# Performance work log

Hardware: AMD Instinct MI355X
Metric: run time of the kernel (lower is better)

## Reference

```python
import jax, jax.numpy as jnp
import numpy as np

DROPOUT = 0.1      # ban radius in normalized coords
INVALID = -2.0     # PositionGetter.INVALID sentinel
EPS = 1e-08


def setup_inputs() -> dict:
    key = jax.random.key(0)
    k1, k2, k3 = jax.random.split(key, 3)
    B, C, T, D = 64, 275, 3000, 2
    x = jax.random.normal(k1, (B, C, T), dtype=jnp.float32)
    positions = jax.random.uniform(k2, (B, C, D), dtype=jnp.float32)
    # row 0: the ban center applied to x; rows 1..100: Monte-Carlo test centers
    centers = jax.random.uniform(k3, (101, D), dtype=jnp.float32)
    return {"x": x, "positions": positions, "centers": centers}


def reference(x, positions, centers):
    # valid_mask: channel is valid unless all coords equal the INVALID sentinel
    valid = ~jnp.all(positions == INVALID, axis=-1)          # [B, C] bool
    x = x * valid[..., None].astype(x.dtype)
    # distances from every channel position to every center, all at once
    # centers: [N, D], positions: [B, C, D] -> dist: [N, B, C]
    diff = positions[None, :, :, :] - centers[:, None, None, :]
    dist = jnp.linalg.norm(diff, axis=-1)                    # [N, B, C]
    kept_all = (dist > DROPOUT) | (~valid)[None]             # [N, B, C] bool
    # apply the actual ban (first center)
    x = x * kept_all[0][..., None].astype(x.dtype)
    # Monte-Carlo keep probability over the remaining 100 centers
    prob_kept = jnp.mean(kept_all[1:].astype(x.dtype), axis=0)  # [B, C]
    return x / (prob_kept[..., None] + EPS)
```

## Files before the change

kernel.cpp:

```cpp
#include <hip/hip_runtime.h>
#include <math.h>


__global__ __launch_bounds__(256) void ChannelDropout_14851996910142_kernel(
    const float* __restrict__ x,
    const float* __restrict__ pos,
    const float* __restrict__ centers,
    float* __restrict__ out,
    int ncenters, int tlen)
{
    const int row = blockIdx.x;
    const int tid = threadIdx.x;
    __shared__ float s_scale;

    if (tid < 64) {
        const float px = pos[2 * row];
        const float py = pos[2 * row + 1];
        const bool valid = !(px == -2.0f && py == -2.0f);

        float cnt = 0.0f;
        for (int c = 1 + tid; c < ncenters; c += 64) {
            const float dx = px - centers[2 * c];
            const float dy = py - centers[2 * c + 1];
            const float d2 = __fadd_rn(__fmul_rn(dx, dx), __fmul_rn(dy, dy));
            const float d = sqrtf(d2);
            cnt += (d > 0.1f) ? 1.0f : 0.0f;
        }
        #pragma unroll
        for (int off = 32; off > 0; off >>= 1)
            cnt += __shfl_down(cnt, off, 64);

        if (tid == 0) {
            const float dx0 = px - centers[0];
            const float dy0 = py - centers[1];
            const float d02 = __fadd_rn(__fmul_rn(dx0, dx0), __fmul_rn(dy0, dy0));
            const bool kept0 = sqrtf(d02) > 0.1f;
            const float prob = cnt / (float)(ncenters - 1);
            s_scale = (valid && kept0) ? (1.0f / (prob + 1e-8f)) : 0.0f;
        }
    }
    __syncthreads();
    const float s = s_scale;

    const size_t base = (size_t)row * (size_t)tlen;
    const int t4 = tlen >> 2;
    const float4* __restrict__ xr = (const float4*)(x + base);
    float4* __restrict__ orow = (float4*)(out + base);
    for (int i = tid; i < t4; i += 256) {
        float4 v = xr[i];
        v.x *= s; v.y *= s; v.z *= s; v.w *= s;
        orow[i] = v;
    }
    for (int i = (t4 << 2) + tid; i < tlen; i += 256) {
        out[base + i] = x[base + i] * s;
    }
}

extern "C" void kernel_launch(void* const* d_in, const int* in_sizes, int n_in,
                              void* d_out, int out_size, void* d_ws, size_t ws_size,
                              hipStream_t stream) {
    const float* x       = (const float*)d_in[0];
    const float* pos     = (const float*)d_in[1];
    const float* centers = (const float*)d_in[2];
    float* out = (float*)d_out;

    const int rows     = in_sizes[1] / 2;
    const int tlen     = in_sizes[0] / rows;
    const int ncenters = in_sizes[2] / 2;

    ChannelDropout_14851996910142_kernel<<<rows, 256, 0, stream>>>(
        x, pos, centers, out, ncenters, tlen);
}
```

Baseline: 348.8 us.

## Split scale computation into separate kernel and use nontemporal streaming loads/stores

Per-row scale computation moves into a small pre-kernel where each thread handles one row and reads the centers from shared memory. The streaming kernel then only loads one precomputed scale per row, so the wave-level reduction and block barrier leave the bandwidth-bound loop. The loop also switches to nontemporal loads and stores to avoid polluting the cache. The cost is a second launch and a workspace round-trip, and the shared buffer caps centers at 256.

```diff
diff --git a/kernel.cpp b/kernel.cpp
--- a/kernel.cpp
+++ b/kernel.cpp
@@ -2,56 +2,63 @@
 #include <math.h>
 
 
-__global__ __launch_bounds__(256) void ChannelDropout_14851996910142_kernel(
-    const float* __restrict__ x,
+typedef float vfloat4 __attribute__((ext_vector_type(4)));
+
+#define MAX_CENTER_FLOATS 512
+
+__global__ __launch_bounds__(256) void ChannelDropout_scale_kernel(
     const float* __restrict__ pos,
     const float* __restrict__ centers,
+    float* __restrict__ scale,
+    int rows, int ncenters)
+{
+    __shared__ float sc[MAX_CENTER_FLOATS];
+    const int nfl = 2 * ncenters;
+    for (int i = threadIdx.x; i < nfl; i += 256) sc[i] = centers[i];
+    __syncthreads();
+
+    const int row = blockIdx.x * 256 + threadIdx.x;
+    if (row >= rows) return;
+
+    const float px = pos[2 * row];
+    const float py = pos[2 * row + 1];
+    const bool valid = !(px == -2.0f && py == -2.0f);
+
+    float cnt = 0.0f;
+    for (int c = 1; c < ncenters; ++c) {
+        const float dx = px - sc[2 * c];
+        const float dy = py - sc[2 * c + 1];
+        const float d = sqrtf(__fadd_rn(__fmul_rn(dx, dx), __fmul_rn(dy, dy)));
+        cnt += (d > 0.1f) ? 1.0f : 0.0f;
+    }
+    const float dx0 = px - sc[0];
+    const float dy0 = py - sc[1];
+    const bool kept0 =
+        sqrtf(__fadd_rn(__fmul_rn(dx0, dx0), __fmul_rn(dy0, dy0))) > 0.1f;
+    const float prob = cnt / (float)(ncenters - 1);
+    scale[row] = (valid && kept0) ? (1.0f / (prob + 1e-8f)) : 0.0f;
+}
+
+__global__ __launch_bounds__(256) void ChannelDropout_apply_kernel(
+    const float* __restrict__ x,
+    const float* __restrict__ scale,
     float* __restrict__ out,
-    int ncenters, int tlen)
+    int tlen)
 {
     const int row = blockIdx.x;
-    const int tid = threadIdx.x;
-    __shared__ float s_scale;
-
-    if (tid < 64) {
-        const float px = pos[2 * row];
-        const float py = pos[2 * row + 1];
-        const bool valid = !(px == -2.0f && py == -2.0f);
-
-        float cnt = 0.0f;
-        for (int c = 1 + tid; c < ncenters; c += 64) {
-            const float dx = px - centers[2 * c];
-            const float dy = py - centers[2 * c + 1];
-            const float d2 = __fadd_rn(__fmul_rn(dx, dx), __fmul_rn(dy, dy));
-            const float d = sqrtf(d2);
-            cnt += (d > 0.1f) ? 1.0f : 0.0f;
-        }
-        #pragma unroll
-        for (int off = 32; off > 0; off >>= 1)
-            cnt += __shfl_down(cnt, off, 64);
-
-        if (tid == 0) {
-            const float dx0 = px - centers[0];
-            const float dy0 = py - centers[1];
-            const float d02 = __fadd_rn(__fmul_rn(dx0, dx0), __fmul_rn(dy0, dy0));
-            const bool kept0 = sqrtf(d02) > 0.1f;
-            const float prob = cnt / (float)(ncenters - 1);
-            s_scale = (valid && kept0) ? (1.0f / (prob + 1e-8f)) : 0.0f;
-        }
-    }
-    __syncthreads();
-    const float s = s_scale;
+    const float s = scale[row];
 
     const size_t base = (size_t)row * (size_t)tlen;
     const int t4 = tlen >> 2;
-    const float4* __restrict__ xr = (const float4*)(x + base);
-    float4* __restrict__ orow = (float4*)(out + base);
-    for (int i = tid; i < t4; i += 256) {
-        float4 v = xr[i];
-        v.x *= s; v.y *= s; v.z *= s; v.w *= s;
-        orow[i] = v;
+    const vfloat4* __restrict__ xr = (const vfloat4*)(x + base);
+    vfloat4* __restrict__ orow = (vfloat4*)(out + base);
+
+    for (int i = threadIdx.x; i < t4; i += 256) {
+        vfloat4 v = __builtin_nontemporal_load(&xr[i]);
+        v *= s;
+        __builtin_nontemporal_store(v, &orow[i]);
     }
-    for (int i = (t4 << 2) + tid; i < tlen; i += 256) {
+    for (int i = (t4 << 2) + (int)threadIdx.x; i < tlen; i += 256) {
         out[base + i] = x[base + i] * s;
     }
 }
@@ -63,11 +70,15 @@
     const float* pos     = (const float*)d_in[1];
     const float* centers = (const float*)d_in[2];
     float* out = (float*)d_out;
+    float* scale = (float*)d_ws;
 
     const int rows     = in_sizes[1] / 2;
     const int tlen     = in_sizes[0] / rows;
     const int ncenters = in_sizes[2] / 2;
 
-    ChannelDropout_14851996910142_kernel<<<rows, 256, 0, stream>>>(
-        x, pos, centers, out, ncenters, tlen);
+    const int sblocks = (rows + 255) / 256;
+    ChannelDropout_scale_kernel<<<sblocks, 256, 0, stream>>>(
+        pos, centers, scale, rows, ncenters);
+    ChannelDropout_apply_kernel<<<rows, 256, 0, stream>>>(
+        x, scale, out, tlen);
 }
```

Result: no change. 349.6 us (+0.2%).
